# Kernel tuning notes

Hardware: AMD Instinct MI355X
Metric: run time of the kernel (lower is better)

Reference implementation:

```python
import jax, jax.numpy as jnp
import numpy as np

N = 100000   # nodes
E = 1600000  # edges (avg degree 16)
D = 128      # input_dim == hidden_dim
H = 128
L = 3        # n_layers
G = 512      # num graphs in batch
LATENT = 64
BN_EPS = 1e-5
SLOPE = 0.2  # LeakyReLU negative slope


def setup_inputs() -> dict:
    key = jax.random.key(0)
    ks = jax.random.split(key, 12)
    s = 1.0 / np.sqrt(H)
    return {
        "x": jax.random.normal(ks[0], (N, D), jnp.float32),
        "edge_index": jax.random.randint(ks[1], (2, E), 0, N, dtype=jnp.int32),
        "batch": jnp.sort(jax.random.randint(ks[2], (N,), 0, G, dtype=jnp.int32)),
        "W1": jax.random.normal(ks[3], (L, D, H), jnp.float32) * s,
        "b1": jax.random.normal(ks[4], (L, H), jnp.float32) * 0.01,
        "g1": jnp.ones((L, H), jnp.float32),
        "beta1": jnp.zeros((L, H), jnp.float32),
        "rm1": jnp.zeros((L, H), jnp.float32),
        "rv1": jnp.ones((L, H), jnp.float32),
        "W2": jax.random.normal(ks[5], (L, H, H), jnp.float32) * s,
        "b2": jax.random.normal(ks[6], (L, H), jnp.float32) * 0.01,
        "bn_g": jnp.ones((H,), jnp.float32),
        "bn_b": jnp.zeros((H,), jnp.float32),
        "bn_rm": jnp.zeros((H,), jnp.float32),
        "bn_rv": jnp.ones((H,), jnp.float32),
        "fcW": jax.random.normal(ks[7], (H, LATENT), jnp.float32) * s,
        "fcb": jax.random.normal(ks[8], (LATENT,), jnp.float32) * 0.01,
    }


def _bn_eval(t, g, b, rm, rv):
    # BatchNorm1d in eval mode: normalize by running stats
    return g * (t - rm) * jax.lax.rsqrt(rv + BN_EPS) + b


def reference(x, edge_index, batch, W1, b1, g1, beta1, rm1, rv1, W2, b2,
              bn_g, bn_b, bn_rm, bn_rv, fcW, fcb):
    src, dst = edge_index[0], edge_index[1]
    h = x
    for i in range(L):
        # GINConv (eps=0): h_i <- MLP(h_i + sum_{j->i} h_j)
        agg = jax.ops.segment_sum(h[src], dst, num_segments=N)
        t = (h + agg) @ W1[i] + b1[i]
        t = jax.nn.leaky_relu(t, SLOPE)
        t = _bn_eval(t, g1[i], beta1[i], rm1[i], rv1[i])
        t = t @ W2[i] + b2[i]
        h = jax.nn.leaky_relu(t, SLOPE)
        # dropout: identity in eval mode
    # global add pool by graph id -> [G, H]
    pooled = jax.ops.segment_sum(h, batch, num_segments=G)
    pooled = _bn_eval(pooled, bn_g, bn_b, bn_rm, bn_rv)
    return pooled @ fcW + fcb
```

## Files before the change

kernel.cpp:

```cpp
#include <hip/hip_runtime.h>

#define NN 100000
#define EE 1600000
#define DD 128
#define HH 128
#define LL 3
#define GG 512
#define LATENT 64
#define BN_EPS 1e-5f
#define SLOPE 0.2f
#define ASTR 136
#define NC (2 * NN)
#define NB_SCAN2 782

typedef __attribute__((ext_vector_type(8))) short short8;
typedef __attribute__((ext_vector_type(4))) float floatx4;

__device__ __forceinline__ float leaky(float t) { return t > 0.f ? t : SLOPE * t; }

__device__ __forceinline__ unsigned short f2bf(float x) {
    union { float f; unsigned int u; } v; v.f = x;
    unsigned int r = v.u + 0x7fffu + ((v.u >> 16) & 1u);
    return (unsigned short)(r >> 16);
}
__device__ __forceinline__ float bf_lo(unsigned int p) {
    union { unsigned int u; float f; } v; v.u = p << 16; return v.f;
}
__device__ __forceinline__ float bf_hi(unsigned int p) {
    union { unsigned int u; float f; } v; v.u = p & 0xffff0000u; return v.f;
}


__global__ void hist2_kernel(const int* __restrict__ dst, int* __restrict__ deg2, int* __restrict__ rank) {
    int e = blockIdx.x * blockDim.x + threadIdx.x;
    if (e < EE) rank[e] = atomicAdd(&deg2[(dst[e] << 1) | (e & 1)], 1);
}

__global__ __launch_bounds__(256) void scan1(const int* __restrict__ deg2, int* __restrict__ bsum) {
    __shared__ int lds[256];
    int n = blockIdx.x * 256 + threadIdx.x;
    lds[threadIdx.x] = (n < NC) ? deg2[n] : 0;
    __syncthreads();
    for (int off = 128; off > 0; off >>= 1) {
        if (threadIdx.x < off) lds[threadIdx.x] += lds[threadIdx.x + off];
        __syncthreads();
    }
    if (threadIdx.x == 0) bsum[blockIdx.x] = lds[0];
}

__global__ __launch_bounds__(1024) void scan2(int* bsum, int* row_ptr2) {
    __shared__ int lds[1024];
    int tid = threadIdx.x;
    int v = (tid < NB_SCAN2) ? bsum[tid] : 0;
    lds[tid] = v;
    __syncthreads();
    for (int off = 1; off < 1024; off <<= 1) {
        int t = (tid >= off) ? lds[tid - off] : 0;
        __syncthreads();
        lds[tid] += t;
        __syncthreads();
    }
    int inc = lds[tid];
    if (tid < NB_SCAN2) bsum[tid] = inc - v;
    if (tid == NB_SCAN2 - 1) row_ptr2[NC] = inc;
}

__global__ __launch_bounds__(256) void scan3(const int* __restrict__ deg2, const int* __restrict__ bsumEx,
                                             int* __restrict__ row_ptr2) {
    __shared__ int lds[256];
    int tid = threadIdx.x;
    int n = blockIdx.x * 256 + tid;
    int v = (n < NC) ? deg2[n] : 0;
    lds[tid] = v;
    __syncthreads();
    for (int off = 1; off < 256; off <<= 1) {
        int t = (tid >= off) ? lds[tid - off] : 0;
        __syncthreads();
        lds[tid] += t;
        __syncthreads();
    }
    int ex = lds[tid] - v;
    if (n < NC) row_ptr2[n] = bsumEx[blockIdx.x] + ex;
}

__global__ void fill2(const int* __restrict__ src, const int* __restrict__ dst,
                      const int* __restrict__ rank, const int* __restrict__ row_ptr2,
                      int* __restrict__ col) {
    int e = blockIdx.x * blockDim.x + threadIdx.x;
    if (e < EE) col[row_ptr2[(dst[e] << 1) | (e & 1)] + rank[e]] = src[e];
}

#define PREP_GS 391
#define PREP_W  (PREP_GS + 48)
__global__ __launch_bounds__(256) void prep_kernel(const int* __restrict__ batch, int* __restrict__ gstart,
                                                   const float* __restrict__ W1, const float* __restrict__ W2,
                                                   uint4* __restrict__ Wf,
                                                   const float2* __restrict__ x2, unsigned int* __restrict__ hx) {
    int b = blockIdx.x;
    if (b < PREP_GS) {
        int n = b * 256 + threadIdx.x;
        if (n >= NN) return;
        int bb = batch[n];
        int pb = (n == 0) ? -1 : batch[n - 1];
        for (int g = pb + 1; g <= bb; ++g) gstart[g] = n;
        if (n == NN - 1)
            for (int g = bb + 1; g <= GG; ++g) gstart[g] = NN;
    } else if (b < PREP_W) {
        int t = (b - PREP_GS) * 256 + threadIdx.x;
        int mat = t >> 11;
        int idx = t & 2047;
        const float* W = ((mat & 1) ? W2 : W1) + (size_t)(mat >> 1) * 128 * 128;
        int lane = idx & 63;
        int tn = (idx >> 6) & 7;
        int kk = idx >> 9;
        int n = tn * 16 + (lane & 15);
        int kb = kk * 32 + (lane >> 4) * 8;
        unsigned int p[4];
#pragma unroll
        for (int jj = 0; jj < 4; ++jj) {
            unsigned short lo = f2bf(W[(kb + 2 * jj) * 128 + n]);
            unsigned short hi = f2bf(W[(kb + 2 * jj + 1) * 128 + n]);
            p[jj] = (unsigned int)lo | ((unsigned int)hi << 16);
        }
        Wf[t] = make_uint4(p[0], p[1], p[2], p[3]);
    } else {
        int i = (b - PREP_W) * 256 + threadIdx.x;
        if (i >= NN * 64) return;
        float2 v = x2[i];
        hx[i] = (unsigned int)f2bf(v.x) | ((unsigned int)f2bf(v.y) << 16);
    }
}
#define PREP_BLOCKS (PREP_W + (NN * 64 + 255) / 256)

__global__ __launch_bounds__(256) void agg_bf16w8(const unsigned int* __restrict__ h,
                                                  const int* __restrict__ row_ptr2,
                                                  const int* __restrict__ col,
                                                  unsigned int* __restrict__ u) {
    int node = blockIdx.x * 4 + (threadIdx.x >> 6);
    int lane = threadIdx.x & 63;
    if (node >= NN) return;
    const int grp = lane >> 3;
    const int sub = lane & 7;
    const uint4* hv = (const uint4*)h;

    float a[16] = {};
    if (grp == 0) {
        uint4 v0 = hv[(size_t)node * 16 + sub];
        uint4 v1 = hv[(size_t)node * 16 + 8 + sub];
        a[0] += bf_lo(v0.x); a[1] += bf_hi(v0.x);
        a[2] += bf_lo(v0.y); a[3] += bf_hi(v0.y);
        a[4] += bf_lo(v0.z); a[5] += bf_hi(v0.z);
        a[6] += bf_lo(v0.w); a[7] += bf_hi(v0.w);
        a[8] += bf_lo(v1.x); a[9] += bf_hi(v1.x);
        a[10] += bf_lo(v1.y); a[11] += bf_hi(v1.y);
        a[12] += bf_lo(v1.z); a[13] += bf_hi(v1.z);
        a[14] += bf_lo(v1.w); a[15] += bf_hi(v1.w);
    }
    int s = row_ptr2[node << 1], e = row_ptr2[(node << 1) + 2];
    for (int j = s + grp; j < e; j += 8) {
        int c = col[j];
        uint4 v0 = hv[(size_t)c * 16 + sub];
        uint4 v1 = hv[(size_t)c * 16 + 8 + sub];
        a[0] += bf_lo(v0.x); a[1] += bf_hi(v0.x);
        a[2] += bf_lo(v0.y); a[3] += bf_hi(v0.y);
        a[4] += bf_lo(v0.z); a[5] += bf_hi(v0.z);
        a[6] += bf_lo(v0.w); a[7] += bf_hi(v0.w);
        a[8] += bf_lo(v1.x); a[9] += bf_hi(v1.x);
        a[10] += bf_lo(v1.y); a[11] += bf_hi(v1.y);
        a[12] += bf_lo(v1.z); a[13] += bf_hi(v1.z);
        a[14] += bf_lo(v1.w); a[15] += bf_hi(v1.w);
    }
#pragma unroll
    for (int t = 0; t < 16; ++t) {
        a[t] += __shfl_xor(a[t], 8);
        a[t] += __shfl_xor(a[t], 16);
        a[t] += __shfl_xor(a[t], 32);
    }
    if (grp == 0) {
        uint4 o0, o1;
        o0.x = (unsigned int)f2bf(a[0]) | ((unsigned int)f2bf(a[1]) << 16);
        o0.y = (unsigned int)f2bf(a[2]) | ((unsigned int)f2bf(a[3]) << 16);
        o0.z = (unsigned int)f2bf(a[4]) | ((unsigned int)f2bf(a[5]) << 16);
        o0.w = (unsigned int)f2bf(a[6]) | ((unsigned int)f2bf(a[7]) << 16);
        o1.x = (unsigned int)f2bf(a[8]) | ((unsigned int)f2bf(a[9]) << 16);
        o1.y = (unsigned int)f2bf(a[10]) | ((unsigned int)f2bf(a[11]) << 16);
        o1.z = (unsigned int)f2bf(a[12]) | ((unsigned int)f2bf(a[13]) << 16);
        o1.w = (unsigned int)f2bf(a[14]) | ((unsigned int)f2bf(a[15]) << 16);
        ((uint4*)u)[(size_t)node * 16 + sub] = o0;
        ((uint4*)u)[(size_t)node * 16 + 8 + sub] = o1;
    }
}

__global__ __launch_bounds__(256) void mlp_fused(const unsigned short* __restrict__ A,
                                                 const uint4* __restrict__ W1f,
                                                 const uint4* __restrict__ W2f,
                                                 const float* __restrict__ b1,
                                                 const float* __restrict__ g,
                                                 const float* __restrict__ beta,
                                                 const float* __restrict__ rm,
                                                 const float* __restrict__ rv,
                                                 const float* __restrict__ b2,
                                                 unsigned short* __restrict__ Out) {
    __shared__ unsigned short aL[128 * ASTR];
    __shared__ unsigned short mL[4][32 * ASTR];
    const int tid = threadIdx.x;
    const int rb = blockIdx.x * 128;

    const uint4* Ag = (const uint4*)(A + (size_t)rb * 128);
#pragma unroll
    for (int it = 0; it < 8; ++it) {
        int idx = it * 256 + tid;
        int r = idx >> 4, c = idx & 15;
        uint4 v = make_uint4(0u, 0u, 0u, 0u);
        if (rb + r < NN) v = Ag[idx];
        *(uint4*)&aL[r * ASTR + c * 8] = v;
    }
    __syncthreads();

    const int wid = tid >> 6, lane = tid & 63;
    const int ml = lane & 15, q = lane >> 4;
    const int m0 = wid * 32;

    floatx4 acc[2][8] = {};
#pragma unroll
    for (int kk = 0; kk < 4; ++kk) {
        short8 af[2];
#pragma unroll
        for (int t = 0; t < 2; ++t)
            af[t] = *(const short8*)&aL[(m0 + t * 16 + ml) * ASTR + kk * 32 + q * 8];
#pragma unroll
        for (int tn = 0; tn < 8; ++tn) {
            uint4 bq = W1f[(kk * 8 + tn) * 64 + lane];
            short8 bf = *(short8*)&bq;
            acc[0][tn] = __builtin_amdgcn_mfma_f32_16x16x32_bf16(af[0], bf, acc[0][tn], 0, 0, 0);
            acc[1][tn] = __builtin_amdgcn_mfma_f32_16x16x32_bf16(af[1], bf, acc[1][tn], 0, 0, 0);
        }
    }

#pragma unroll
    for (int tn = 0; tn < 8; ++tn) {
        int c = tn * 16 + ml;
        float s = g[c] * rsqrtf(rv[c] + BN_EPS);
        float sh = beta[c] - s * rm[c];
        float bv = b1[c];
#pragma unroll
        for (int t = 0; t < 2; ++t)
#pragma unroll
            for (int r = 0; r < 4; ++r) {
                float val = leaky(acc[t][tn][r] + bv);
                val = s * val + sh;
                mL[wid][(t * 16 + q * 4 + r) * ASTR + c] = f2bf(val);
            }
    }
    __syncthreads();

    floatx4 acc2[2][8] = {};
#pragma unroll
    for (int kk = 0; kk < 4; ++kk) {
        short8 af[2];
#pragma unroll
        for (int t = 0; t < 2; ++t)
            af[t] = *(const short8*)&mL[wid][(t * 16 + ml) * ASTR + kk * 32 + q * 8];
#pragma unroll
        for (int tn = 0; tn < 8; ++tn) {
            uint4 bq = W2f[(kk * 8 + tn) * 64 + lane];
            short8 bf = *(short8*)&bq;
            acc2[0][tn] = __builtin_amdgcn_mfma_f32_16x16x32_bf16(af[0], bf, acc2[0][tn], 0, 0, 0);
            acc2[1][tn] = __builtin_amdgcn_mfma_f32_16x16x32_bf16(af[1], bf, acc2[1][tn], 0, 0, 0);
        }
    }

#pragma unroll
    for (int tn = 0; tn < 8; ++tn) {
        int c = tn * 16 + ml;
        float bv = b2[c];
#pragma unroll
        for (int t = 0; t < 2; ++t)
#pragma unroll
            for (int r = 0; r < 4; ++r) {
                int row = rb + m0 + t * 16 + q * 4 + r;
                if (row < NN)
                    Out[(size_t)row * 128 + c] = f2bf(leaky(acc2[t][tn][r] + bv));
            }
    }
}

__global__ __launch_bounds__(256) void pool_bf16(const unsigned int* __restrict__ h,
                                                 const int* __restrict__ gstart,
                                                 const float* __restrict__ bng,
                                                 const float* __restrict__ bnb,
                                                 const float* __restrict__ bnrm,
                                                 const float* __restrict__ bnrv,
                                                 float* __restrict__ pooled) {
    __shared__ float lds[4][128];
    int g = blockIdx.x;
    int wid = threadIdx.x >> 6, lane = threadIdx.x & 63;
    int s = gstart[g], e = gstart[g + 1];
    float ax = 0.f, ay = 0.f;
    for (int n = s + wid; n < e; n += 4) {
        unsigned int v = h[(size_t)n * 64 + lane];
        ax += bf_lo(v);
        ay += bf_hi(v);
    }
    lds[wid][lane * 2] = ax;
    lds[wid][lane * 2 + 1] = ay;
    __syncthreads();
    if (wid == 0) {
#pragma unroll
        for (int t = 0; t < 2; ++t) {
            int c = lane * 2 + t;
            float acc = lds[0][c] + lds[1][c] + lds[2][c] + lds[3][c];
            pooled[g * 128 + c] = bng[c] * (acc - bnrm[c]) * rsqrtf(bnrv[c] + BN_EPS) + bnb[c];
        }
    }
}

__global__ __launch_bounds__(64) void final_kernel(const float* __restrict__ pooled,
                                                   const float* __restrict__ fcW,
                                                   const float* __restrict__ fcb,
                                                   float* __restrict__ out) {
    int g = blockIdx.x;
    int l = threadIdx.x;
    float acc = fcb[l];
#pragma unroll 8
    for (int c = 0; c < HH; ++c) acc += pooled[g * 128 + c] * fcW[c * LATENT + l];
    out[g * LATENT + l] = acc;
}

extern "C" void kernel_launch(void* const* d_in, const int* in_sizes, int n_in,
                              void* d_out, int out_size, void* d_ws, size_t ws_size,
                              hipStream_t stream) {
    const float* x = (const float*)d_in[0];
    const int* ei = (const int*)d_in[1];
    const int* batch = (const int*)d_in[2];
    const float* W1 = (const float*)d_in[3];
    const float* b1 = (const float*)d_in[4];
    const float* g1 = (const float*)d_in[5];
    const float* beta1 = (const float*)d_in[6];
    const float* rm1 = (const float*)d_in[7];
    const float* rv1 = (const float*)d_in[8];
    const float* W2 = (const float*)d_in[9];
    const float* b2 = (const float*)d_in[10];
    const float* bn_g = (const float*)d_in[11];
    const float* bn_b = (const float*)d_in[12];
    const float* bn_rm = (const float*)d_in[13];
    const float* bn_rv = (const float*)d_in[14];
    const float* fcW = (const float*)d_in[15];
    const float* fcb = (const float*)d_in[16];
    float* out = (float*)d_out;

    const int* src = ei;
    const int* dst = ei + EE;

    char* w = (char*)d_ws;
    size_t off = 0;
    auto alloc = [&](size_t bytes) -> char* {
        char* p = w + off;
        off += (bytes + 1023) & ~(size_t)1023;
        return p;
    };
    unsigned int* hx = (unsigned int*)alloc(4 * (size_t)NN * 64);
    unsigned int* ubuf = (unsigned int*)alloc(4 * (size_t)NN * 64);
    unsigned int* hbuf = (unsigned int*)alloc(4 * (size_t)NN * 64);
    uint4* Wf = (uint4*)alloc(16 * (size_t)6 * 2048);
    int* deg2 = (int*)alloc(4 * (size_t)NC);
    int* row_ptr2 = (int*)alloc(4 * (size_t)(NC + 1));
    int* rank = (int*)alloc(4 * (size_t)EE);
    int* col = (int*)alloc(4 * (size_t)EE);
    int* bsum = (int*)alloc(4 * 1024);
    int* gstart = (int*)alloc(4 * (GG + 1));
    float* pooled = (float*)alloc(sizeof(float) * GG * 128);
    (void)ws_size; (void)in_sizes; (void)n_in; (void)out_size;

    hipMemsetAsync(deg2, 0, 4 * (size_t)NC, stream);
    hist2_kernel<<<(EE + 255) / 256, 256, 0, stream>>>(dst, deg2, rank);
    scan1<<<NB_SCAN2, 256, 0, stream>>>(deg2, bsum);
    scan2<<<1, 1024, 0, stream>>>(bsum, row_ptr2);
    scan3<<<NB_SCAN2, 256, 0, stream>>>(deg2, bsum, row_ptr2);
    fill2<<<(EE + 255) / 256, 256, 0, stream>>>(src, dst, rank, row_ptr2, col);

    prep_kernel<<<PREP_BLOCKS, 256, 0, stream>>>(batch, gstart, W1, W2, Wf, (const float2*)x, hx);

    const int gblocks = (NN + 127) / 128;
    const unsigned int* hcur = hx;
    for (int i = 0; i < LL; ++i) {
        agg_bf16w8<<<(NN + 3) / 4, 256, 0, stream>>>(hcur, row_ptr2, col, ubuf);
        mlp_fused<<<gblocks, 256, 0, stream>>>((const unsigned short*)ubuf,
                                               Wf + (size_t)(2 * i) * 2048,
                                               Wf + (size_t)(2 * i + 1) * 2048,
                                               b1 + i * HH, g1 + i * HH, beta1 + i * HH,
                                               rm1 + i * HH, rv1 + i * HH, b2 + i * HH,
                                               (unsigned short*)hbuf);
        hcur = hbuf;
    }
    pool_bf16<<<GG, 256, 0, stream>>>(hbuf, gstart, bn_g, bn_b, bn_rm, bn_rv, pooled);
    final_kernel<<<GG, 64, 0, stream>>>(pooled, fcW, fcb, out);
}
```

Before: 555.2 us.

## Merge preprocessing kernels, drop scan2 with per-block prefix, fuse pool and FC

Folds the histogram atomics and the prep work (graph starts, weight packing, bf16 conversion of x) into a single launch. The conversion now handles eight floats per thread instead of two. The separate single-block scan2 is removed: each scan3f block sums all earlier block totals itself, and the final row pointer is written as the known edge count. Pooling and the final FC layer are fused into one kernel that keeps the pooled row in LDS, and the aggregation accumulators are switched to float2 vectors. The aim is fewer kernel launches and less launch overhead, at the cost of redundant prefix summing of up to 782 block totals per scan block.

```diff
diff --git a/kernel.cpp b/kernel.cpp
--- a/kernel.cpp
+++ b/kernel.cpp
@@ -11,10 +11,11 @@
 #define SLOPE 0.2f
 #define ASTR 136
 #define NC (2 * NN)
-#define NB_SCAN2 782
+#define NB2 782
 
 typedef __attribute__((ext_vector_type(8))) short short8;
 typedef __attribute__((ext_vector_type(4))) float floatx4;
+typedef __attribute__((ext_vector_type(2))) float floatx2;
 
 __device__ __forceinline__ float leaky(float t) { return t > 0.f ? t : SLOPE * t; }
 
@@ -23,90 +24,54 @@
     unsigned int r = v.u + 0x7fffu + ((v.u >> 16) & 1u);
     return (unsigned short)(r >> 16);
 }
+__device__ __forceinline__ unsigned int pk2(float a, float b) {
+    return (unsigned int)f2bf(a) | ((unsigned int)f2bf(b) << 16);
+}
 __device__ __forceinline__ float bf_lo(unsigned int p) {
     union { unsigned int u; float f; } v; v.u = p << 16; return v.f;
 }
 __device__ __forceinline__ float bf_hi(unsigned int p) {
     union { unsigned int u; float f; } v; v.u = p & 0xffff0000u; return v.f;
 }
-
-
-__global__ void hist2_kernel(const int* __restrict__ dst, int* __restrict__ deg2, int* __restrict__ rank) {
-    int e = blockIdx.x * blockDim.x + threadIdx.x;
-    if (e < EE) rank[e] = atomicAdd(&deg2[(dst[e] << 1) | (e & 1)], 1);
-}
-
-__global__ __launch_bounds__(256) void scan1(const int* __restrict__ deg2, int* __restrict__ bsum) {
-    __shared__ int lds[256];
-    int n = blockIdx.x * 256 + threadIdx.x;
-    lds[threadIdx.x] = (n < NC) ? deg2[n] : 0;
-    __syncthreads();
-    for (int off = 128; off > 0; off >>= 1) {
-        if (threadIdx.x < off) lds[threadIdx.x] += lds[threadIdx.x + off];
-        __syncthreads();
-    }
-    if (threadIdx.x == 0) bsum[blockIdx.x] = lds[0];
-}
-
-__global__ __launch_bounds__(1024) void scan2(int* bsum, int* row_ptr2) {
-    __shared__ int lds[1024];
+__device__ __forceinline__ floatx2 up2(unsigned int p) {
+    union { unsigned int u; float f; } lo, hi;
+    lo.u = p << 16; hi.u = p & 0xffff0000u;
+    floatx2 r; r.x = lo.f; r.y = hi.f; return r;
+}
+
+#define HIST_B 6250
+#define PG 391
+#define PW 48
+#define PX 6250
+#define HP_BLOCKS (HIST_B + PG + PW + PX)
+
+__global__ __launch_bounds__(256) void histprep(const int* __restrict__ dst,
+                                                int* __restrict__ deg2, int* __restrict__ rank,
+                                                const int* __restrict__ batch, int* __restrict__ gstart,
+                                                const float* __restrict__ W1, const float* __restrict__ W2,
+                                                uint4* __restrict__ Wf,
+                                                const float4* __restrict__ x4, uint4* __restrict__ hx4) {
+    int b = blockIdx.x;
     int tid = threadIdx.x;
-    int v = (tid < NB_SCAN2) ? bsum[tid] : 0;
-    lds[tid] = v;
-    __syncthreads();
-    for (int off = 1; off < 1024; off <<= 1) {
-        int t = (tid >= off) ? lds[tid - off] : 0;
-        __syncthreads();
-        lds[tid] += t;
-        __syncthreads();
-    }
-    int inc = lds[tid];
-    if (tid < NB_SCAN2) bsum[tid] = inc - v;
-    if (tid == NB_SCAN2 - 1) row_ptr2[NC] = inc;
-}
-
-__global__ __launch_bounds__(256) void scan3(const int* __restrict__ deg2, const int* __restrict__ bsumEx,
-                                             int* __restrict__ row_ptr2) {
-    __shared__ int lds[256];
-    int tid = threadIdx.x;
-    int n = blockIdx.x * 256 + tid;
-    int v = (n < NC) ? deg2[n] : 0;
-    lds[tid] = v;
-    __syncthreads();
-    for (int off = 1; off < 256; off <<= 1) {
-        int t = (tid >= off) ? lds[tid - off] : 0;
-        __syncthreads();
-        lds[tid] += t;
-        __syncthreads();
-    }
-    int ex = lds[tid] - v;
-    if (n < NC) row_ptr2[n] = bsumEx[blockIdx.x] + ex;
-}
-
-__global__ void fill2(const int* __restrict__ src, const int* __restrict__ dst,
-                      const int* __restrict__ rank, const int* __restrict__ row_ptr2,
-                      int* __restrict__ col) {
-    int e = blockIdx.x * blockDim.x + threadIdx.x;
-    if (e < EE) col[row_ptr2[(dst[e] << 1) | (e & 1)] + rank[e]] = src[e];
-}
-
-#define PREP_GS 391
-#define PREP_W  (PREP_GS + 48)
-__global__ __launch_bounds__(256) void prep_kernel(const int* __restrict__ batch, int* __restrict__ gstart,
-                                                   const float* __restrict__ W1, const float* __restrict__ W2,
-                                                   uint4* __restrict__ Wf,
-                                                   const float2* __restrict__ x2, unsigned int* __restrict__ hx) {
-    int b = blockIdx.x;
-    if (b < PREP_GS) {
-        int n = b * 256 + threadIdx.x;
+    if (b < HIST_B) {
+        int e = b * 256 + tid;
+        if (e < EE) rank[e] = atomicAdd(&deg2[(dst[e] << 1) | (e & 1)], 1);
+        return;
+    }
+    b -= HIST_B;
+    if (b < PG) {
+        int n = b * 256 + tid;
         if (n >= NN) return;
         int bb = batch[n];
         int pb = (n == 0) ? -1 : batch[n - 1];
         for (int g = pb + 1; g <= bb; ++g) gstart[g] = n;
         if (n == NN - 1)
             for (int g = bb + 1; g <= GG; ++g) gstart[g] = NN;
-    } else if (b < PREP_W) {
-        int t = (b - PREP_GS) * 256 + threadIdx.x;
+        return;
+    }
+    b -= PG;
+    if (b < PW) {
+        int t = b * 256 + tid;
         int mat = t >> 11;
         int idx = t & 2047;
         const float* W = ((mat & 1) ? W2 : W1) + (size_t)(mat >> 1) * 128 * 128;
@@ -117,20 +82,70 @@
         int kb = kk * 32 + (lane >> 4) * 8;
         unsigned int p[4];
 #pragma unroll
-        for (int jj = 0; jj < 4; ++jj) {
-            unsigned short lo = f2bf(W[(kb + 2 * jj) * 128 + n]);
-            unsigned short hi = f2bf(W[(kb + 2 * jj + 1) * 128 + n]);
-            p[jj] = (unsigned int)lo | ((unsigned int)hi << 16);
-        }
+        for (int jj = 0; jj < 4; ++jj)
+            p[jj] = pk2(W[(kb + 2 * jj) * 128 + n], W[(kb + 2 * jj + 1) * 128 + n]);
         Wf[t] = make_uint4(p[0], p[1], p[2], p[3]);
-    } else {
-        int i = (b - PREP_W) * 256 + threadIdx.x;
-        if (i >= NN * 64) return;
-        float2 v = x2[i];
-        hx[i] = (unsigned int)f2bf(v.x) | ((unsigned int)f2bf(v.y) << 16);
-    }
-}
-#define PREP_BLOCKS (PREP_W + (NN * 64 + 255) / 256)
+        return;
+    }
+    b -= PW;
+    int i = b * 256 + tid;
+    if (i >= NN * 16) return;
+    float4 p0 = x4[2 * i], p1 = x4[2 * i + 1];
+    uint4 o;
+    o.x = pk2(p0.x, p0.y);
+    o.y = pk2(p0.z, p0.w);
+    o.z = pk2(p1.x, p1.y);
+    o.w = pk2(p1.z, p1.w);
+    hx4[i] = o;
+}
+
+__global__ __launch_bounds__(256) void scan1(const int* __restrict__ deg2, int* __restrict__ bsum) {
+    __shared__ int lds[256];
+    int n = blockIdx.x * 256 + threadIdx.x;
+    lds[threadIdx.x] = (n < NC) ? deg2[n] : 0;
+    __syncthreads();
+    for (int off = 128; off > 0; off >>= 1) {
+        if (threadIdx.x < off) lds[threadIdx.x] += lds[threadIdx.x + off];
+        __syncthreads();
+    }
+    if (threadIdx.x == 0) bsum[blockIdx.x] = lds[0];
+}
+
+__global__ __launch_bounds__(256) void scan3f(const int* __restrict__ deg2, const int* __restrict__ bsum,
+                                              int* __restrict__ row_ptr2) {
+    __shared__ int red[256];
+    int tid = threadIdx.x;
+    int bid = blockIdx.x;
+    int acc = 0;
+    for (int j = tid; j < bid; j += 256) acc += bsum[j];
+    red[tid] = acc;
+    __syncthreads();
+    for (int off = 128; off > 0; off >>= 1) {
+        if (tid < off) red[tid] += red[tid + off];
+        __syncthreads();
+    }
+    int base = red[0];
+    __syncthreads();
+    int n = bid * 256 + tid;
+    int v = (n < NC) ? deg2[n] : 0;
+    red[tid] = v;
+    __syncthreads();
+    for (int off = 1; off < 256; off <<= 1) {
+        int t = (tid >= off) ? red[tid - off] : 0;
+        __syncthreads();
+        red[tid] += t;
+        __syncthreads();
+    }
+    if (n < NC) row_ptr2[n] = base + red[tid] - v;
+    if (n == 0) row_ptr2[NC] = EE;
+}
+
+__global__ void fill2(const int* __restrict__ src, const int* __restrict__ dst,
+                      const int* __restrict__ rank, const int* __restrict__ row_ptr2,
+                      int* __restrict__ col) {
+    int e = blockIdx.x * blockDim.x + threadIdx.x;
+    if (e < EE) col[row_ptr2[(dst[e] << 1) | (e & 1)] + rank[e]] = src[e];
+}
 
 __global__ __launch_bounds__(256) void agg_bf16w8(const unsigned int* __restrict__ h,
                                                   const int* __restrict__ row_ptr2,
@@ -143,49 +158,43 @@
     const int sub = lane & 7;
     const uint4* hv = (const uint4*)h;
 
-    float a[16] = {};
+    floatx2 a[8];
+#pragma unroll
+    for (int t = 0; t < 8; ++t) { a[t].x = 0.f; a[t].y = 0.f; }
+
     if (grp == 0) {
         uint4 v0 = hv[(size_t)node * 16 + sub];
         uint4 v1 = hv[(size_t)node * 16 + 8 + sub];
-        a[0] += bf_lo(v0.x); a[1] += bf_hi(v0.x);
-        a[2] += bf_lo(v0.y); a[3] += bf_hi(v0.y);
-        a[4] += bf_lo(v0.z); a[5] += bf_hi(v0.z);
-        a[6] += bf_lo(v0.w); a[7] += bf_hi(v0.w);
-        a[8] += bf_lo(v1.x); a[9] += bf_hi(v1.x);
-        a[10] += bf_lo(v1.y); a[11] += bf_hi(v1.y);
-        a[12] += bf_lo(v1.z); a[13] += bf_hi(v1.z);
-        a[14] += bf_lo(v1.w); a[15] += bf_hi(v1.w);
+        a[0] += up2(v0.x); a[1] += up2(v0.y); a[2] += up2(v0.z); a[3] += up2(v0.w);
+        a[4] += up2(v1.x); a[5] += up2(v1.y); a[6] += up2(v1.z); a[7] += up2(v1.w);
     }
     int s = row_ptr2[node << 1], e = row_ptr2[(node << 1) + 2];
     for (int j = s + grp; j < e; j += 8) {
         int c = col[j];
         uint4 v0 = hv[(size_t)c * 16 + sub];
         uint4 v1 = hv[(size_t)c * 16 + 8 + sub];
-        a[0] += bf_lo(v0.x); a[1] += bf_hi(v0.x);
-        a[2] += bf_lo(v0.y); a[3] += bf_hi(v0.y);
-        a[4] += bf_lo(v0.z); a[5] += bf_hi(v0.z);
-        a[6] += bf_lo(v0.w); a[7] += bf_hi(v0.w);
-        a[8] += bf_lo(v1.x); a[9] += bf_hi(v1.x);
-        a[10] += bf_lo(v1.y); a[11] += bf_hi(v1.y);
-        a[12] += bf_lo(v1.z); a[13] += bf_hi(v1.z);
-        a[14] += bf_lo(v1.w); a[15] += bf_hi(v1.w);
-    }
-#pragma unroll
-    for (int t = 0; t < 16; ++t) {
-        a[t] += __shfl_xor(a[t], 8);
-        a[t] += __shfl_xor(a[t], 16);
-        a[t] += __shfl_xor(a[t], 32);
+        a[0] += up2(v0.x); a[1] += up2(v0.y); a[2] += up2(v0.z); a[3] += up2(v0.w);
+        a[4] += up2(v1.x); a[5] += up2(v1.y); a[6] += up2(v1.z); a[7] += up2(v1.w);
+    }
+#pragma unroll
+    for (int t = 0; t < 8; ++t) {
+        a[t].x += __shfl_xor(a[t].x, 8);
+        a[t].y += __shfl_xor(a[t].y, 8);
+        a[t].x += __shfl_xor(a[t].x, 16);
+        a[t].y += __shfl_xor(a[t].y, 16);
+        a[t].x += __shfl_xor(a[t].x, 32);
+        a[t].y += __shfl_xor(a[t].y, 32);
     }
     if (grp == 0) {
         uint4 o0, o1;
-        o0.x = (unsigned int)f2bf(a[0]) | ((unsigned int)f2bf(a[1]) << 16);
-        o0.y = (unsigned int)f2bf(a[2]) | ((unsigned int)f2bf(a[3]) << 16);
-        o0.z = (unsigned int)f2bf(a[4]) | ((unsigned int)f2bf(a[5]) << 16);
-        o0.w = (unsigned int)f2bf(a[6]) | ((unsigned int)f2bf(a[7]) << 16);
-        o1.x = (unsigned int)f2bf(a[8]) | ((unsigned int)f2bf(a[9]) << 16);
-        o1.y = (unsigned int)f2bf(a[10]) | ((unsigned int)f2bf(a[11]) << 16);
-        o1.z = (unsigned int)f2bf(a[12]) | ((unsigned int)f2bf(a[13]) << 16);
-        o1.w = (unsigned int)f2bf(a[14]) | ((unsigned int)f2bf(a[15]) << 16);
+        o0.x = pk2(a[0].x, a[0].y);
+        o0.y = pk2(a[1].x, a[1].y);
+        o0.z = pk2(a[2].x, a[2].y);
+        o0.w = pk2(a[3].x, a[3].y);
+        o1.x = pk2(a[4].x, a[4].y);
+        o1.y = pk2(a[5].x, a[5].y);
+        o1.z = pk2(a[6].x, a[6].y);
+        o1.w = pk2(a[7].x, a[7].y);
         ((uint4*)u)[(size_t)node * 16 + sub] = o0;
         ((uint4*)u)[(size_t)node * 16 + 8 + sub] = o1;
     }
@@ -285,16 +294,20 @@
     }
 }
 
-__global__ __launch_bounds__(256) void pool_bf16(const unsigned int* __restrict__ h,
-                                                 const int* __restrict__ gstart,
-                                                 const float* __restrict__ bng,
-                                                 const float* __restrict__ bnb,
-                                                 const float* __restrict__ bnrm,
-                                                 const float* __restrict__ bnrv,
-                                                 float* __restrict__ pooled) {
+__global__ __launch_bounds__(256) void poolfc(const unsigned int* __restrict__ h,
+                                              const int* __restrict__ gstart,
+                                              const float* __restrict__ bng,
+                                              const float* __restrict__ bnb,
+                                              const float* __restrict__ bnrm,
+                                              const float* __restrict__ bnrv,
+                                              const float* __restrict__ fcW,
+                                              const float* __restrict__ fcb,
+                                              float* __restrict__ out) {
     __shared__ float lds[4][128];
+    __shared__ float pcol[128];
     int g = blockIdx.x;
-    int wid = threadIdx.x >> 6, lane = threadIdx.x & 63;
+    int tid = threadIdx.x;
+    int wid = tid >> 6, lane = tid & 63;
     int s = gstart[g], e = gstart[g + 1];
     float ax = 0.f, ay = 0.f;
     for (int n = s + wid; n < e; n += 4) {
@@ -305,26 +318,17 @@
     lds[wid][lane * 2] = ax;
     lds[wid][lane * 2 + 1] = ay;
     __syncthreads();
-    if (wid == 0) {
-#pragma unroll
-        for (int t = 0; t < 2; ++t) {
-            int c = lane * 2 + t;
-            float acc = lds[0][c] + lds[1][c] + lds[2][c] + lds[3][c];
-            pooled[g * 128 + c] = bng[c] * (acc - bnrm[c]) * rsqrtf(bnrv[c] + BN_EPS) + bnb[c];
-        }
-    }
-}
-
-__global__ __launch_bounds__(64) void final_kernel(const float* __restrict__ pooled,
-                                                   const float* __restrict__ fcW,
-                                                   const float* __restrict__ fcb,
-                                                   float* __restrict__ out) {
-    int g = blockIdx.x;
-    int l = threadIdx.x;
-    float acc = fcb[l];
+    if (tid < 128) {
+        float acc = lds[0][tid] + lds[1][tid] + lds[2][tid] + lds[3][tid];
+        pcol[tid] = bng[tid] * (acc - bnrm[tid]) * rsqrtf(bnrv[tid] + BN_EPS) + bnb[tid];
+    }
+    __syncthreads();
+    if (tid < LATENT) {
+        float acc = fcb[tid];
 #pragma unroll 8
-    for (int c = 0; c < HH; ++c) acc += pooled[g * 128 + c] * fcW[c * LATENT + l];
-    out[g * LATENT + l] = acc;
+        for (int c = 0; c < HH; ++c) acc += pcol[c] * fcW[c * LATENT + tid];
+        out[g * LATENT + tid] = acc;
+    }
 }
 
 extern "C" void kernel_launch(void* const* d_in, const int* in_sizes, int n_in,
@@ -369,17 +373,14 @@
     int* col = (int*)alloc(4 * (size_t)EE);
     int* bsum = (int*)alloc(4 * 1024);
     int* gstart = (int*)alloc(4 * (GG + 1));
-    float* pooled = (float*)alloc(sizeof(float) * GG * 128);
     (void)ws_size; (void)in_sizes; (void)n_in; (void)out_size;
 
     hipMemsetAsync(deg2, 0, 4 * (size_t)NC, stream);
-    hist2_kernel<<<(EE + 255) / 256, 256, 0, stream>>>(dst, deg2, rank);
-    scan1<<<NB_SCAN2, 256, 0, stream>>>(deg2, bsum);
-    scan2<<<1, 1024, 0, stream>>>(bsum, row_ptr2);
-    scan3<<<NB_SCAN2, 256, 0, stream>>>(deg2, bsum, row_ptr2);
+    histprep<<<HP_BLOCKS, 256, 0, stream>>>(dst, deg2, rank, batch, gstart,
+                                            W1, W2, Wf, (const float4*)x, (uint4*)hx);
+    scan1<<<NB2, 256, 0, stream>>>(deg2, bsum);
+    scan3f<<<NB2, 256, 0, stream>>>(deg2, bsum, row_ptr2);
     fill2<<<(EE + 255) / 256, 256, 0, stream>>>(src, dst, rank, row_ptr2, col);
-
-    prep_kernel<<<PREP_BLOCKS, 256, 0, stream>>>(batch, gstart, W1, W2, Wf, (const float2*)x, hx);
 
     const int gblocks = (NN + 127) / 128;
     const unsigned int* hcur = hx;
@@ -393,6 +394,5 @@
                                                (unsigned short*)hbuf);
         hcur = hbuf;
     }
-    pool_bf16<<<GG, 256, 0, stream>>>(hbuf, gstart, bn_g, bn_b, bn_rm, bn_rv, pooled);
-    final_kernel<<<GG, 64, 0, stream>>>(pooled, fcW, fcb, out);
-}
+    poolfc<<<GG, 256, 0, stream>>>(hbuf, gstart, bn_g, bn_b, bn_rm, bn_rv, fcW, fcb, out);
+}
```

Result: no change. 548.5 us (-1.2%).
